# Kernel optimization log

Measured on AMD Instinct MI355X. Metric: run time of the kernel, lower is better.

## Reference

```python
import jax, jax.numpy as jnp
import numpy as np
import math

PATCH = 41
NUM_ANG = 8
NUM_SPATIAL = 4
BIN_KSIZE = 2 * int(PATCH / (NUM_SPATIAL + 1))   # 16
BIN_STRIDE = PATCH // NUM_SPATIAL                # 10
BIN_PAD = BIN_KSIZE // 4                         # 4
CLIPVAL = 0.2
EPS = 1e-10
N = 8192


def _sift_pooling_kernel(ksize: int) -> np.ndarray:
    k2 = float(ksize) / 2.0
    xc2 = k2 - np.abs(np.arange(ksize, dtype=np.float32) + 0.5 - k2)
    return (np.outer(xc2, xc2) / k2 ** 2).astype(np.float32)


def _sift_weighting_kernel(ksize: int) -> np.ndarray:
    # Gauss, vlfeat sigma: sigma_mul_2 = ksize**2
    k2 = float(ksize) / 2.0
    ys = np.arange(ksize, dtype=np.float32)[:, None]
    xs = np.arange(ksize, dtype=np.float32)[None, :]
    disq = (ys - k2 + 0.5) ** 2 + (xs - k2 + 0.5) ** 2
    return np.exp(-disq / float(ksize ** 2)).astype(np.float32)


def setup_inputs() -> dict:
    key = jax.random.key(0)
    x = jax.random.normal(key, (N, 1, PATCH, PATCH), dtype=jnp.float32)
    gk = jnp.asarray(_sift_weighting_kernel(PATCH))   # [41,41]
    pk = jnp.asarray(_sift_pooling_kernel(BIN_KSIZE))  # [16,16]
    return {"x": x, "gk": gk, "pk": pk}


def _l2_normalize(v):
    return v / jnp.maximum(jnp.linalg.norm(v, axis=1, keepdims=True), 1e-12)


def reference(x, gk, pk):
    # gradients via replicate-pad + central difference (matches [-1,0,1] convs)
    xp = jnp.pad(x, ((0, 0), (0, 0), (0, 0), (1, 1)), mode='edge')
    gx = xp[..., 2:] - xp[..., :-2]
    yp = jnp.pad(x, ((0, 0), (0, 0), (1, 1), (0, 0)), mode='edge')
    gy = yp[:, :, 2:, :] - yp[:, :, :-2, :]

    mag = jnp.sqrt(gx * gx + gy * gy + EPS) * gk  # gaussian-weighted magnitude
    ori = jnp.arctan2(gy, gx + EPS)

    # soft angular binning
    o_big = (ori + 2.0 * math.pi) / (2.0 * math.pi) * NUM_ANG
    bo0f = jnp.floor(o_big)
    wo1 = o_big - bo0f
    bo0 = bo0f.astype(jnp.int32) % NUM_ANG
    bo1 = (bo0 + 1) % NUM_ANG
    # [N,1,P,P,nb]
    contrib = (jax.nn.one_hot(bo0, NUM_ANG, dtype=mag.dtype) * ((1.0 - wo1) * mag)[..., None]
               + jax.nn.one_hot(bo1, NUM_ANG, dtype=mag.dtype) * (wo1 * mag)[..., None])
    contrib = jnp.transpose(contrib[:, 0], (0, 3, 1, 2))  # [N,nb,P,P]

    # depthwise weighted spatial pooling (same triangular kernel per angular bin)
    kern = jnp.broadcast_to(pk[None, None], (NUM_ANG, 1, BIN_KSIZE, BIN_KSIZE))
    pooled = jax.lax.conv_general_dilated(
        contrib, kern,
        window_strides=(BIN_STRIDE, BIN_STRIDE),
        padding=[(BIN_PAD, BIN_PAD), (BIN_PAD, BIN_PAD)],
        feature_group_count=NUM_ANG,
        dimension_numbers=('NCHW', 'OIHW', 'NCHW'))  # [N,nb,4,4]

    desc = pooled.reshape(pooled.shape[0], -1)  # [N,128]
    desc = _l2_normalize(desc)
    desc = jnp.clip(desc, 0.0, CLIPVAL)
    desc = _l2_normalize(desc)
    # rootsift: sqrt of L1-normalized descriptor
    desc = desc / jnp.maximum(jnp.sum(jnp.abs(desc), axis=1, keepdims=True), 1e-12)
    return jnp.sqrt(desc + 1e-10)
```

## Files before the change

### kernel.cpp

```cpp
#include <hip/hip_runtime.h>
#include <hip/hip_fp16.h>
#include <math.h>

#define PATCH 41
#define PP 1681
#define NB 8
#define STRIDE 10
#define NTH 192
#define HR 5
#define PPB 4
#define TAIL (PP - 8 * NTH)

__device__ __forceinline__ constexpr float tri16(int k) {
    float d = (float)k + 0.5f - 8.0f;
    float a = d < 0.0f ? -d : d;
    return (8.0f - a) * 0.125f;
}

__device__ __forceinline__ uint4 pixel_contrib(float gx, float gy, float w) {
    float X = gx + 1e-10f;
    float mag = __builtin_amdgcn_sqrtf(fmaf(gx, gx, fmaf(gy, gy, 1e-10f))) * w;

    float ax = fabsf(X), ay = fabsf(gy);
    float mx = fmaxf(ax, ay), mn = fminf(ax, ay);
    float r = mn * __builtin_amdgcn_rcpf(fmaxf(mx, 1e-30f));
    float r2 = r * r;
    float a4 = fmaf(r2, -0.0149238f, 0.0670406f);
    a4 = fmaf(r2, a4, -0.1482457f);
    a4 = fmaf(r2, a4, 0.2464287f);
    a4 = fmaf(r2, a4, -0.4235106f);
    a4 = fmaf(r2, a4, 1.2732106f);
    a4 *= r;

    bool sw = ay > ax;
    bool xn = X < 0.0f;
    bool yn = gy < 0.0f;
    int q = (xn ? 2 : 0) + ((sw != xn) ? 1 : 0);
    int b0 = yn ? 7 - q : q;
    bool f = (sw != xn) != yn;
    float ma = a4 * mag;
    float mb = mag - ma;
    float v0 = f ? ma : mb;
    float v1 = f ? mb : ma;

    unsigned combo = __builtin_bit_cast(unsigned, __builtin_amdgcn_cvt_pkrtz(v0, v1));
    int sh = (b0 & 3) << 4;
    unsigned long long A = (unsigned long long)combo << sh;
    unsigned long long B = ((b0 & 3) == 3) ? (unsigned long long)(combo >> 16) : 0ull;
    bool lohalf = b0 < 4;
    unsigned long long lo = lohalf ? A : B;
    unsigned long long hi = lohalf ? B : A;
    uint4 cw;
    cw.x = (unsigned)lo; cw.y = (unsigned)(lo >> 32);
    cw.z = (unsigned)hi; cw.w = (unsigned)(hi >> 32);
    return cw;
}

__device__ __forceinline__ __half2 u2h2(unsigned v) {
    return __builtin_bit_cast(__half2, v);
}

__device__ __forceinline__ unsigned dpp_prev(unsigned v) {
    return (unsigned)__builtin_amdgcn_update_dpp(0, (int)v, 0x111, 0xF, 0xF, true);
}
__device__ __forceinline__ unsigned dpp_next(unsigned v) {
    return (unsigned)__builtin_amdgcn_update_dpp(0, (int)v, 0x101, 0xF, 0xF, true);
}

__global__ __launch_bounds__(NTH, 6) void sift_desc_kernel(
        const float* __restrict__ x,
        const float* __restrict__ gk,
        const float* __restrict__ pk,
        float* __restrict__ out,
        int n)
{
    const int t = threadIdx.x;
    const int base = blockIdx.x * PPB;

    __shared__ __align__(16) float sA[PP];
    __shared__ __align__(16) float sB[PP];
    __shared__ __align__(16) __half s_H[49 * HR * NB];

    if (t < 160) {
        int dw = (t < 80) ? t : (820 + t);
        ((unsigned*)s_H)[dw] = 0u;
    }

    const int row = t >> 2;
    const int ox  = t & 3;
    const int cb  = ox * STRIDE;
    const bool ox0 = (ox == 0);
    const bool ox3 = (ox == 3);
    const float drow = (float)(row - 20);
    const float rf = __builtin_amdgcn_exp2f(drow * drow * -8.582362e-4f);
    const __half2 z2 = __float2half2_rn(0.0f);
    const __half2 wl[4] = {
        ox0 ? z2 : __float2half2_rn(tri16(0)),
        ox0 ? z2 : __float2half2_rn(tri16(1)),
        ox0 ? z2 : __float2half2_rn(tri16(2)),
        ox0 ? z2 : __float2half2_rn(tri16(3))
    };
    const int rb = row * PATCH + cb;
    const int ru = (row > 0 ? row - 1 : 0) * PATCH + cb;
    const int rd = (row < PATCH - 1 ? row + 1 : PATCH - 1) * PATCH + cb;

    float w[11];
    #pragma unroll
    for (int i = 0; i < 11; ++i) {
        float dc = (float)(cb + i - 20);
        w[i] = __builtin_amdgcn_exp2f(dc * dc * -8.582362e-4f) * rf;
    }

    {
        const float* gp = x + (size_t)base * PP;
        float stg[9];
        #pragma unroll
        for (int it = 0; it < 8; ++it) stg[it] = gp[it * NTH + t];
        stg[8] = (t < TAIL) ? gp[8 * NTH + t] : 0.0f;
        #pragma unroll
        for (int it = 0; it < 8; ++it) sA[it * NTH + t] = stg[it];
        if (t < TAIL) sA[8 * NTH + t] = stg[8];
    }
    __syncthreads();

    #pragma unroll
    for (int pi = 0; pi < PPB; ++pi) {
        if (base + pi >= n) break;
        const float* sC = (pi & 1) ? sB : sA;
        float*       sN = (pi & 1) ? sA : sB;
        const bool hn = (pi + 1 < PPB) && (base + pi + 1 < n);

        float stg[9];
        if (hn) {
            const float* gp = x + (size_t)(base + pi + 1) * PP;
            #pragma unroll
            for (int it = 0; it < 8; ++it) stg[it] = gp[it * NTH + t];
            stg[8] = (t < TAIL) ? gp[8 * NTH + t] : 0.0f;
        }
        __builtin_amdgcn_sched_barrier(0);

        if (t < PATCH * 4) {
            float m[13], u[11], d[11];
            m[0]  = sC[rb + (ox0 ? 0 : -1)];
            #pragma unroll
            for (int i = 1; i < 12; ++i) m[i] = sC[rb + i - 1];
            m[12] = sC[rb + (ox3 ? 10 : 11)];
            #pragma unroll
            for (int i = 0; i < 11; ++i) u[i] = sC[ru + i];
            #pragma unroll
            for (int i = 0; i < 11; ++i) d[i] = sC[rd + i];

            __half2 a0 = z2, a1 = z2, a2 = z2, a3 = z2;

            #pragma unroll
            for (int k = 0; k <= 10; ++k) {
                uint4 cw = pixel_contrib(m[k + 2] - m[k], d[k] - u[k], w[k]);

                const __half2 wo = __float2half2_rn(tri16(k + 4));
                a0 = __hfma2(u2h2(cw.x), wo, a0);
                a1 = __hfma2(u2h2(cw.y), wo, a1);
                a2 = __hfma2(u2h2(cw.z), wo, a2);
                a3 = __hfma2(u2h2(cw.w), wo, a3);

                if (k == 1) {
                    unsigned rx = dpp_next(cw.x);
                    unsigned ry = dpp_next(cw.y);
                    unsigned rz = dpp_next(cw.z);
                    unsigned rw = dpp_next(cw.w);
                    rx = ox3 ? 0u : rx;  ry = ox3 ? 0u : ry;
                    rz = ox3 ? 0u : rz;  rw = ox3 ? 0u : rw;
                    const __half2 wr = __float2half2_rn(tri16(15));
                    a0 = __hfma2(u2h2(rx), wr, a0);
                    a1 = __hfma2(u2h2(ry), wr, a1);
                    a2 = __hfma2(u2h2(rz), wr, a2);
                    a3 = __hfma2(u2h2(rw), wr, a3);
                }
                if (k >= 6 && k < 10) {
                    const __half2 wk = wl[k - 6];
                    a0 = __hfma2(u2h2(dpp_prev(cw.x)), wk, a0);
                    a1 = __hfma2(u2h2(dpp_prev(cw.y)), wk, a1);
                    a2 = __hfma2(u2h2(dpp_prev(cw.z)), wk, a2);
                    a3 = __hfma2(u2h2(dpp_prev(cw.w)), wk, a3);
                }
            }

            uint4 hv;
            hv.x = __builtin_bit_cast(unsigned, a0);
            hv.y = __builtin_bit_cast(unsigned, a1);
            hv.z = __builtin_bit_cast(unsigned, a2);
            hv.w = __builtin_bit_cast(unsigned, a3);
            *(uint4*)&s_H[((row + 4) * HR + ox) * NB] = hv;
        }
        __syncthreads();

        if (hn) {
            #pragma unroll
            for (int it = 0; it < 8; ++it) sN[it * NTH + t] = stg[it];
            if (t < TAIL) sN[8 * NTH + t] = stg[8];
        }

        if (t < 64) {
            const int b   = t >> 4;
            const int oy  = (t >> 2) & 3;
            const int oxx = t & 3;
            const __half* hp = &s_H[(oy * STRIDE * HR + oxx) * NB + b];
            float a = 0.0f, bb = 0.0f;
            #pragma unroll
            for (int ky = 0; ky < 16; ++ky) {
                a  = fmaf(tri16(ky), __half2float(hp[ky * HR * NB]),     a);
                bb = fmaf(tri16(ky), __half2float(hp[ky * HR * NB + 4]), bb);
            }

            float ss = fmaf(a, a, bb * bb);
            #pragma unroll
            for (int o = 32; o > 0; o >>= 1) ss += __shfl_xor(ss, o);
            float inv = 1.0f / fmaxf(__builtin_amdgcn_sqrtf(ss), 1e-12f);
            a  = fminf(fmaxf(a * inv, 0.0f), 0.2f);
            bb = fminf(fmaxf(bb * inv, 0.0f), 0.2f);

            float ss2 = fmaf(a, a, bb * bb);
            #pragma unroll
            for (int o = 32; o > 0; o >>= 1) ss2 += __shfl_xor(ss2, o);
            float inv2 = 1.0f / fmaxf(__builtin_amdgcn_sqrtf(ss2), 1e-12f);
            a *= inv2; bb *= inv2;

            float l1 = a + bb;
            #pragma unroll
            for (int o = 32; o > 0; o >>= 1) l1 += __shfl_xor(l1, o);
            float invl = 1.0f / fmaxf(l1, 1e-12f);

            float* op = out + (size_t)(base + pi) * 128;
            op[t]      = __builtin_amdgcn_sqrtf(fmaf(a,  invl, 1e-10f));
            op[t + 64] = __builtin_amdgcn_sqrtf(fmaf(bb, invl, 1e-10f));
        }
        __syncthreads();
    }
}

extern "C" void kernel_launch(void* const* d_in, const int* in_sizes, int n_in,
                              void* d_out, int out_size, void* d_ws, size_t ws_size,
                              hipStream_t stream) {
    const float* x  = (const float*)d_in[0];
    const float* gk = (const float*)d_in[1];
    const float* pk = (const float*)d_in[2];
    float* out = (float*)d_out;
    const int n = in_sizes[0] / PP;
    const int grid = (n + PPB - 1) / PPB;
    sift_desc_kernel<<<grid, NTH, 0, stream>>>(x, gk, pk, out, n);
}
```

Baseline: 111.7 us.

## Assign one wavefront per patch and remove block-wide barriers

Each 64-lane wavefront now owns a whole patch, with three patches per 192-thread block. Each wave loops three times to cover the 164 row/column work items, and the block-wide __syncthreads calls and the cross-patch double-buffered prefetch are gone. The Gaussian column weights now come from a small LDS table instead of per-thread exp2 calls, and launch bounds drop from 6 to 3. The aim is to cut barrier stalls and idle threads during the normalization stage. The cost is losing explicit load/compute overlap within a block and using more LDS per block, which may reduce occupancy.

```diff
diff --git a/kernel.cpp b/kernel.cpp
--- a/kernel.cpp
+++ b/kernel.cpp
@@ -8,8 +8,6 @@
 #define STRIDE 10
 #define NTH 192
 #define HR 5
-#define PPB 4
-#define TAIL (PP - 8 * NTH)
 
 __device__ __forceinline__ constexpr float tri16(int k) {
     float d = (float)k + 0.5f - 8.0f;
@@ -67,94 +65,88 @@
     return (unsigned)__builtin_amdgcn_update_dpp(0, (int)v, 0x101, 0xF, 0xF, true);
 }
 
-__global__ __launch_bounds__(NTH, 6) void sift_desc_kernel(
+__global__ __launch_bounds__(NTH, 3) void sift_desc_kernel(
         const float* __restrict__ x,
         const float* __restrict__ gk,
         const float* __restrict__ pk,
         float* __restrict__ out,
         int n)
 {
-    const int t = threadIdx.x;
-    const int base = blockIdx.x * PPB;
-
-    __shared__ __align__(16) float sA[PP];
-    __shared__ __align__(16) float sB[PP];
-    __shared__ __align__(16) __half s_H[49 * HR * NB];
-
-    if (t < 160) {
-        int dw = (t < 80) ? t : (820 + t);
-        ((unsigned*)s_H)[dw] = 0u;
-    }
-
-    const int row = t >> 2;
-    const int ox  = t & 3;
-    const int cb  = ox * STRIDE;
-    const bool ox0 = (ox == 0);
-    const bool ox3 = (ox == 3);
-    const float drow = (float)(row - 20);
-    const float rf = __builtin_amdgcn_exp2f(drow * drow * -8.582362e-4f);
+    const int t    = threadIdx.x;
+    const int lane = t & 63;
+    const int wv   = t >> 6;
+    const int patch = blockIdx.x * 3 + wv;
+
+    __shared__ __align__(16) float  sW[3][PP];
+    __shared__ __align__(16) __half sH[3][49 * HR * NB];
+    __shared__ float s_gc[48];
+
+    if (lane < 48) {
+        float dd = (float)(lane - 20);
+        float g = __builtin_amdgcn_exp2f(dd * dd * -8.582362e-4f);
+        s_gc[lane] = (lane < PATCH) ? g : 0.0f;
+    }
+    {
+        unsigned* hz = (unsigned*)&sH[wv][0];
+        #pragma unroll
+        for (int j = 0; j < 3; ++j) {
+            int idx = 64 * j + lane;
+            if (idx < 160) hz[(idx < 80) ? idx : (820 + idx)] = 0u;
+        }
+    }
+    if (patch >= n) return;
+
+    {
+        const float* gp = x + (size_t)patch * PP;
+        float* wp = &sW[wv][0];
+        #pragma unroll
+        for (int i = 0; i < 26; ++i) wp[lane + 64 * i] = gp[lane + 64 * i];
+        if (lane < PP - 26 * 64) wp[lane + 26 * 64] = gp[lane + 26 * 64];
+    }
+
+    const float* sC = &sW[wv][0];
     const __half2 z2 = __float2half2_rn(0.0f);
-    const __half2 wl[4] = {
-        ox0 ? z2 : __float2half2_rn(tri16(0)),
-        ox0 ? z2 : __float2half2_rn(tri16(1)),
-        ox0 ? z2 : __float2half2_rn(tri16(2)),
-        ox0 ? z2 : __float2half2_rn(tri16(3))
-    };
-    const int rb = row * PATCH + cb;
-    const int ru = (row > 0 ? row - 1 : 0) * PATCH + cb;
-    const int rd = (row < PATCH - 1 ? row + 1 : PATCH - 1) * PATCH + cb;
-
-    float w[11];
+
     #pragma unroll
-    for (int i = 0; i < 11; ++i) {
-        float dc = (float)(cb + i - 20);
-        w[i] = __builtin_amdgcn_exp2f(dc * dc * -8.582362e-4f) * rf;
-    }
-
-    {
-        const float* gp = x + (size_t)base * PP;
-        float stg[9];
-        #pragma unroll
-        for (int it = 0; it < 8; ++it) stg[it] = gp[it * NTH + t];
-        stg[8] = (t < TAIL) ? gp[8 * NTH + t] : 0.0f;
-        #pragma unroll
-        for (int it = 0; it < 8; ++it) sA[it * NTH + t] = stg[it];
-        if (t < TAIL) sA[8 * NTH + t] = stg[8];
-    }
-    __syncthreads();
-
-    #pragma unroll
-    for (int pi = 0; pi < PPB; ++pi) {
-        if (base + pi >= n) break;
-        const float* sC = (pi & 1) ? sB : sA;
-        float*       sN = (pi & 1) ? sA : sB;
-        const bool hn = (pi + 1 < PPB) && (base + pi + 1 < n);
-
-        float stg[9];
-        if (hn) {
-            const float* gp = x + (size_t)(base + pi + 1) * PP;
-            #pragma unroll
-            for (int it = 0; it < 8; ++it) stg[it] = gp[it * NTH + t];
-            stg[8] = (t < TAIL) ? gp[8 * NTH + t] : 0.0f;
-        }
-        __builtin_amdgcn_sched_barrier(0);
-
-        if (t < PATCH * 4) {
-            float m[13], u[11], d[11];
+    for (int it = 0; it < 3; ++it) {
+        const int u = 64 * it + lane;
+        if (u < PATCH * 4) {
+            const int row = u >> 2;
+            const int ox  = u & 3;
+            const int cb  = ox * STRIDE;
+            const bool ox0 = (ox == 0);
+            const bool ox3 = (ox == 3);
+            const int rb = row * PATCH + cb;
+            const int ru = (row > 0 ? row - 1 : 0) * PATCH + cb;
+            const int rd = (row < PATCH - 1 ? row + 1 : PATCH - 1) * PATCH + cb;
+
+            const float drow = (float)(row - 20);
+            const float rf = __builtin_amdgcn_exp2f(drow * drow * -8.582362e-4f);
+
+            const __half2 wl[4] = {
+                ox0 ? z2 : __float2half2_rn(tri16(0)),
+                ox0 ? z2 : __float2half2_rn(tri16(1)),
+                ox0 ? z2 : __float2half2_rn(tri16(2)),
+                ox0 ? z2 : __float2half2_rn(tri16(3))
+            };
+
+            float m[13], uu[11], dd[11], w[11];
             m[0]  = sC[rb + (ox0 ? 0 : -1)];
             #pragma unroll
             for (int i = 1; i < 12; ++i) m[i] = sC[rb + i - 1];
             m[12] = sC[rb + (ox3 ? 10 : 11)];
             #pragma unroll
-            for (int i = 0; i < 11; ++i) u[i] = sC[ru + i];
-            #pragma unroll
-            for (int i = 0; i < 11; ++i) d[i] = sC[rd + i];
+            for (int i = 0; i < 11; ++i) uu[i] = sC[ru + i];
+            #pragma unroll
+            for (int i = 0; i < 11; ++i) dd[i] = sC[rd + i];
+            #pragma unroll
+            for (int i = 0; i < 11; ++i) w[i] = s_gc[cb + i] * rf;
 
             __half2 a0 = z2, a1 = z2, a2 = z2, a3 = z2;
 
             #pragma unroll
             for (int k = 0; k <= 10; ++k) {
-                uint4 cw = pixel_contrib(m[k + 2] - m[k], d[k] - u[k], w[k]);
+                uint4 cw = pixel_contrib(m[k + 2] - m[k], dd[k] - uu[k], w[k]);
 
                 const __half2 wo = __float2half2_rn(tri16(k + 4));
                 a0 = __hfma2(u2h2(cw.x), wo, a0);
@@ -189,51 +181,43 @@
             hv.y = __builtin_bit_cast(unsigned, a1);
             hv.z = __builtin_bit_cast(unsigned, a2);
             hv.w = __builtin_bit_cast(unsigned, a3);
-            *(uint4*)&s_H[((row + 4) * HR + ox) * NB] = hv;
+            *(uint4*)&sH[wv][((row + 4) * HR + ox) * NB] = hv;
         }
-        __syncthreads();
-
-        if (hn) {
-            #pragma unroll
-            for (int it = 0; it < 8; ++it) sN[it * NTH + t] = stg[it];
-            if (t < TAIL) sN[8 * NTH + t] = stg[8];
+    }
+
+    {
+        const int b   = lane >> 4;
+        const int oy  = (lane >> 2) & 3;
+        const int oxx = lane & 3;
+        const __half* hp = &sH[wv][(oy * STRIDE * HR + oxx) * NB + b];
+        float a = 0.0f, bb = 0.0f;
+        #pragma unroll
+        for (int ky = 0; ky < 16; ++ky) {
+            a  = fmaf(tri16(ky), __half2float(hp[ky * HR * NB]),     a);
+            bb = fmaf(tri16(ky), __half2float(hp[ky * HR * NB + 4]), bb);
         }
 
-        if (t < 64) {
-            const int b   = t >> 4;
-            const int oy  = (t >> 2) & 3;
-            const int oxx = t & 3;
-            const __half* hp = &s_H[(oy * STRIDE * HR + oxx) * NB + b];
-            float a = 0.0f, bb = 0.0f;
-            #pragma unroll
-            for (int ky = 0; ky < 16; ++ky) {
-                a  = fmaf(tri16(ky), __half2float(hp[ky * HR * NB]),     a);
-                bb = fmaf(tri16(ky), __half2float(hp[ky * HR * NB + 4]), bb);
-            }
-
-            float ss = fmaf(a, a, bb * bb);
-            #pragma unroll
-            for (int o = 32; o > 0; o >>= 1) ss += __shfl_xor(ss, o);
-            float inv = 1.0f / fmaxf(__builtin_amdgcn_sqrtf(ss), 1e-12f);
-            a  = fminf(fmaxf(a * inv, 0.0f), 0.2f);
-            bb = fminf(fmaxf(bb * inv, 0.0f), 0.2f);
-
-            float ss2 = fmaf(a, a, bb * bb);
-            #pragma unroll
-            for (int o = 32; o > 0; o >>= 1) ss2 += __shfl_xor(ss2, o);
-            float inv2 = 1.0f / fmaxf(__builtin_amdgcn_sqrtf(ss2), 1e-12f);
-            a *= inv2; bb *= inv2;
-
-            float l1 = a + bb;
-            #pragma unroll
-            for (int o = 32; o > 0; o >>= 1) l1 += __shfl_xor(l1, o);
-            float invl = 1.0f / fmaxf(l1, 1e-12f);
-
-            float* op = out + (size_t)(base + pi) * 128;
-            op[t]      = __builtin_amdgcn_sqrtf(fmaf(a,  invl, 1e-10f));
-            op[t + 64] = __builtin_amdgcn_sqrtf(fmaf(bb, invl, 1e-10f));
-        }
-        __syncthreads();
+        float ss = fmaf(a, a, bb * bb);
+        #pragma unroll
+        for (int o = 32; o > 0; o >>= 1) ss += __shfl_xor(ss, o);
+        float inv = 1.0f / fmaxf(__builtin_amdgcn_sqrtf(ss), 1e-12f);
+        a  = fminf(fmaxf(a * inv, 0.0f), 0.2f);
+        bb = fminf(fmaxf(bb * inv, 0.0f), 0.2f);
+
+        float ss2 = fmaf(a, a, bb * bb);
+        #pragma unroll
+        for (int o = 32; o > 0; o >>= 1) ss2 += __shfl_xor(ss2, o);
+        float inv2 = 1.0f / fmaxf(__builtin_amdgcn_sqrtf(ss2), 1e-12f);
+        a *= inv2; bb *= inv2;
+
+        float l1 = a + bb;
+        #pragma unroll
+        for (int o = 32; o > 0; o >>= 1) l1 += __shfl_xor(l1, o);
+        float invl = 1.0f / fmaxf(l1, 1e-12f);
+
+        float* op = out + (size_t)patch * 128;
+        op[lane]      = __builtin_amdgcn_sqrtf(fmaf(a,  invl, 1e-10f));
+        op[lane + 64] = __builtin_amdgcn_sqrtf(fmaf(bb, invl, 1e-10f));
     }
 }
 
@@ -245,6 +229,6 @@
     const float* pk = (const float*)d_in[2];
     float* out = (float*)d_out;
     const int n = in_sizes[0] / PP;
-    const int grid = (n + PPB - 1) / PPB;
+    const int grid = (n + 2) / 3;
     sift_desc_kernel<<<grid, NTH, 0, stream>>>(x, gk, pk, out, n);
 }
```

Result: no change. 111.3 us (-0.4%).

## Process two patches per iteration with interleaved contributions and paired pooling

Applied to the files above, without the earlier changes.

Restructures the per-block loop to handle two patches per iteration. sA and sB now hold a pair instead of serving as a ping-pong buffer, and the histogram buffer is duplicated. The per-pixel gradient and binning work for both patches is interleaved to raise ILP, and the final pooling and normalisation runs on two wavefronts at once. This halves the number of barriers per patch. Patches per block double and the occupancy hint drops from 6 to 4 to cover the higher register pressure, which costs latency hiding and leaves fewer blocks (1024 instead of 2048).

```diff
diff --git a/kernel.cpp b/kernel.cpp
--- a/kernel.cpp
+++ b/kernel.cpp
@@ -8,7 +8,7 @@
 #define STRIDE 10
 #define NTH 192
 #define HR 5
-#define PPB 4
+#define PPB 8
 #define TAIL (PP - 8 * NTH)
 
 __device__ __forceinline__ constexpr float tri16(int k) {
@@ -67,7 +67,35 @@
     return (unsigned)__builtin_amdgcn_update_dpp(0, (int)v, 0x101, 0xF, 0xF, true);
 }
 
-__global__ __launch_bounds__(NTH, 6) void sift_desc_kernel(
+#define ACCUM(K, CW, A0, A1, A2, A3) do {                                        \
+    const __half2 wo_ = __float2half2_rn(tri16((K) + 4));                        \
+    A0 = __hfma2(u2h2((CW).x), wo_, A0);                                         \
+    A1 = __hfma2(u2h2((CW).y), wo_, A1);                                         \
+    A2 = __hfma2(u2h2((CW).z), wo_, A2);                                         \
+    A3 = __hfma2(u2h2((CW).w), wo_, A3);                                         \
+    if ((K) == 1) {                                                              \
+        unsigned rx_ = dpp_next((CW).x);                                         \
+        unsigned ry_ = dpp_next((CW).y);                                         \
+        unsigned rz_ = dpp_next((CW).z);                                         \
+        unsigned rw_ = dpp_next((CW).w);                                         \
+        rx_ = ox3 ? 0u : rx_;  ry_ = ox3 ? 0u : ry_;    \
+        rz_ = ox3 ? 0u : rz_;  rw_ = ox3 ? 0u : rw_;                             \
+        const __half2 wr_ = __float2half2_rn(tri16(15));                         \
+        A0 = __hfma2(u2h2(rx_), wr_, A0);                                        \
+        A1 = __hfma2(u2h2(ry_), wr_, A1);                                        \
+        A2 = __hfma2(u2h2(rz_), wr_, A2);                                        \
+        A3 = __hfma2(u2h2(rw_), wr_, A3);                                        \
+    }                                                                            \
+    if ((K) >= 6 && (K) < 10) {      \
+        const __half2 wk_ = wl[(K) - 6];                                         \
+        A0 = __hfma2(u2h2(dpp_prev((CW).x)), wk_, A0);                           \
+        A1 = __hfma2(u2h2(dpp_prev((CW).y)), wk_, A1);                           \
+        A2 = __hfma2(u2h2(dpp_prev((CW).z)), wk_, A2);                           \
+        A3 = __hfma2(u2h2(dpp_prev((CW).w)), wk_, A3);                           \
+    }                                                                            \
+} while (0)
+
+__global__ __launch_bounds__(NTH, 4) void sift_desc_kernel(
         const float* __restrict__ x,
         const float* __restrict__ gk,
         const float* __restrict__ pk,
@@ -79,11 +107,12 @@
 
     __shared__ __align__(16) float sA[PP];
     __shared__ __align__(16) float sB[PP];
-    __shared__ __align__(16) __half s_H[49 * HR * NB];
+    __shared__ __align__(16) __half sH2[2][49 * HR * NB];
 
     if (t < 160) {
         int dw = (t < 80) ? t : (820 + t);
-        ((unsigned*)s_H)[dw] = 0u;
+        ((unsigned*)sH2)[dw] = 0u;
+        ((unsigned*)sH2)[980 + dw] = 0u;
     }
 
     const int row = t >> 2;
@@ -112,126 +141,116 @@
     }
 
     {
-        const float* gp = x + (size_t)base * PP;
-        float stg[9];
+        const float* gA = x + (size_t)base * PP;
+        const float* gB = x + (size_t)min(base + 1, n - 1) * PP;
+        float sa[9], sb[9];
         #pragma unroll
-        for (int it = 0; it < 8; ++it) stg[it] = gp[it * NTH + t];
-        stg[8] = (t < TAIL) ? gp[8 * NTH + t] : 0.0f;
+        for (int it = 0; it < 8; ++it) { sa[it] = gA[it * NTH + t]; sb[it] = gB[it * NTH + t]; }
+        sa[8] = (t < TAIL) ? gA[8 * NTH + t] : 0.0f;
+        sb[8] = (t < TAIL) ? gB[8 * NTH + t] : 0.0f;
         #pragma unroll
-        for (int it = 0; it < 8; ++it) sA[it * NTH + t] = stg[it];
-        if (t < TAIL) sA[8 * NTH + t] = stg[8];
+        for (int it = 0; it < 8; ++it) { sA[it * NTH + t] = sa[it]; sB[it * NTH + t] = sb[it]; }
+        if (t < TAIL) { sA[8 * NTH + t] = sa[8]; sB[8 * NTH + t] = sb[8]; }
     }
     __syncthreads();
 
     #pragma unroll
-    for (int pi = 0; pi < PPB; ++pi) {
-        if (base + pi >= n) break;
-        const float* sC = (pi & 1) ? sB : sA;
-        float*       sN = (pi & 1) ? sA : sB;
-        const bool hn = (pi + 1 < PPB) && (base + pi + 1 < n);
-
-        float stg[9];
+    for (int pp = 0; pp < PPB / 2; ++pp) {
+        const int pairbase = base + 2 * pp;
+        if (pairbase >= n) break;
+        const bool hn = (pp + 1 < PPB / 2) && (pairbase + 2 < n);
+
+        float sa[9], sb[9];
         if (hn) {
-            const float* gp = x + (size_t)(base + pi + 1) * PP;
-            #pragma unroll
-            for (int it = 0; it < 8; ++it) stg[it] = gp[it * NTH + t];
-            stg[8] = (t < TAIL) ? gp[8 * NTH + t] : 0.0f;
+            const float* gA = x + (size_t)(pairbase + 2) * PP;
+            const float* gB = x + (size_t)min(pairbase + 3, n - 1) * PP;
+            #pragma unroll
+            for (int it = 0; it < 8; ++it) { sa[it] = gA[it * NTH + t]; sb[it] = gB[it * NTH + t]; }
+            sa[8] = (t < TAIL) ? gA[8 * NTH + t] : 0.0f;
+            sb[8] = (t < TAIL) ? gB[8 * NTH + t] : 0.0f;
         }
         __builtin_amdgcn_sched_barrier(0);
 
         if (t < PATCH * 4) {
-            float m[13], u[11], d[11];
-            m[0]  = sC[rb + (ox0 ? 0 : -1)];
-            #pragma unroll
-            for (int i = 1; i < 12; ++i) m[i] = sC[rb + i - 1];
-            m[12] = sC[rb + (ox3 ? 10 : 11)];
-            #pragma unroll
-            for (int i = 0; i < 11; ++i) u[i] = sC[ru + i];
-            #pragma unroll
-            for (int i = 0; i < 11; ++i) d[i] = sC[rd + i];
-
-            __half2 a0 = z2, a1 = z2, a2 = z2, a3 = z2;
+            float mA[13], uA[11], dA[11];
+            float mB[13], uB[11], dB[11];
+            mA[0] = sA[rb + (ox0 ? 0 : -1)];   mB[0] = sB[rb + (ox0 ? 0 : -1)];
+            #pragma unroll
+            for (int i = 1; i < 12; ++i) { mA[i] = sA[rb + i - 1]; mB[i] = sB[rb + i - 1]; }
+            mA[12] = sA[rb + (ox3 ? 10 : 11)]; mB[12] = sB[rb + (ox3 ? 10 : 11)];
+            #pragma unroll
+            for (int i = 0; i < 11; ++i) { uA[i] = sA[ru + i]; uB[i] = sB[ru + i]; }
+            #pragma unroll
+            for (int i = 0; i < 11; ++i) { dA[i] = sA[rd + i]; dB[i] = sB[rd + i]; }
+
+            __half2 aA0 = z2, aA1 = z2, aA2 = z2, aA3 = z2;
+            __half2 aB0 = z2, aB1 = z2, aB2 = z2, aB3 = z2;
 
             #pragma unroll
             for (int k = 0; k <= 10; ++k) {
-                uint4 cw = pixel_contrib(m[k + 2] - m[k], d[k] - u[k], w[k]);
-
-                const __half2 wo = __float2half2_rn(tri16(k + 4));
-                a0 = __hfma2(u2h2(cw.x), wo, a0);
-                a1 = __hfma2(u2h2(cw.y), wo, a1);
-                a2 = __hfma2(u2h2(cw.z), wo, a2);
-                a3 = __hfma2(u2h2(cw.w), wo, a3);
-
-                if (k == 1) {
-                    unsigned rx = dpp_next(cw.x);
-                    unsigned ry = dpp_next(cw.y);
-                    unsigned rz = dpp_next(cw.z);
-                    unsigned rw = dpp_next(cw.w);
-                    rx = ox3 ? 0u : rx;  ry = ox3 ? 0u : ry;
-                    rz = ox3 ? 0u : rz;  rw = ox3 ? 0u : rw;
-                    const __half2 wr = __float2half2_rn(tri16(15));
-                    a0 = __hfma2(u2h2(rx), wr, a0);
-                    a1 = __hfma2(u2h2(ry), wr, a1);
-                    a2 = __hfma2(u2h2(rz), wr, a2);
-                    a3 = __hfma2(u2h2(rw), wr, a3);
+                uint4 cwA = pixel_contrib(mA[k + 2] - mA[k], dA[k] - uA[k], w[k]);
+                ACCUM(k, cwA, aA0, aA1, aA2, aA3);
+                uint4 cwB = pixel_contrib(mB[k + 2] - mB[k], dB[k] - uB[k], w[k]);
+                ACCUM(k, cwB, aB0, aB1, aB2, aB3);
+            }
+
+            uint4 hvA, hvB;
+            hvA.x = __builtin_bit_cast(unsigned, aA0);
+            hvA.y = __builtin_bit_cast(unsigned, aA1);
+            hvA.z = __builtin_bit_cast(unsigned, aA2);
+            hvA.w = __builtin_bit_cast(unsigned, aA3);
+            hvB.x = __builtin_bit_cast(unsigned, aB0);
+            hvB.y = __builtin_bit_cast(unsigned, aB1);
+            hvB.z = __builtin_bit_cast(unsigned, aB2);
+            hvB.w = __builtin_bit_cast(unsigned, aB3);
+            *(uint4*)&sH2[0][((row + 4) * HR + ox) * NB] = hvA;
+            *(uint4*)&sH2[1][((row + 4) * HR + ox) * NB] = hvB;
+        }
+        __syncthreads();
+
+        if (hn) {
+            #pragma unroll
+            for (int it = 0; it < 8; ++it) { sA[it * NTH + t] = sa[it]; sB[it * NTH + t] = sb[it]; }
+            if (t < TAIL) { sA[8 * NTH + t] = sa[8]; sB[8 * NTH + t] = sb[8]; }
+        }
+
+        if (t < 128) {
+            const int which = t >> 6;
+            const int lane  = t & 63;
+            if (pairbase + which < n) {
+                const int b   = lane >> 4;
+                const int oy  = (lane >> 2) & 3;
+                const int oxx = lane & 3;
+                const __half* hp = &sH2[which][(oy * STRIDE * HR + oxx) * NB + b];
+                float a = 0.0f, bb = 0.0f;
+                #pragma unroll
+                for (int ky = 0; ky < 16; ++ky) {
+                    a  = fmaf(tri16(ky), __half2float(hp[ky * HR * NB]),     a);
+                    bb = fmaf(tri16(ky), __half2float(hp[ky * HR * NB + 4]), bb);
                 }
-                if (k >= 6 && k < 10) {
-                    const __half2 wk = wl[k - 6];
-                    a0 = __hfma2(u2h2(dpp_prev(cw.x)), wk, a0);
-                    a1 = __hfma2(u2h2(dpp_prev(cw.y)), wk, a1);
-                    a2 = __hfma2(u2h2(dpp_prev(cw.z)), wk, a2);
-                    a3 = __hfma2(u2h2(dpp_prev(cw.w)), wk, a3);
-                }
+
+                float ss = fmaf(a, a, bb * bb);
+                #pragma unroll
+                for (int o = 32; o > 0; o >>= 1) ss += __shfl_xor(ss, o);
+                float inv = 1.0f / fmaxf(__builtin_amdgcn_sqrtf(ss), 1e-12f);
+                a  = fminf(fmaxf(a * inv, 0.0f), 0.2f);
+                bb = fminf(fmaxf(bb * inv, 0.0f), 0.2f);
+
+                float ss2 = fmaf(a, a, bb * bb);
+                #pragma unroll
+                for (int o = 32; o > 0; o >>= 1) ss2 += __shfl_xor(ss2, o);
+                float inv2 = 1.0f / fmaxf(__builtin_amdgcn_sqrtf(ss2), 1e-12f);
+                a *= inv2; bb *= inv2;
+
+                float l1 = a + bb;
+                #pragma unroll
+                for (int o = 32; o > 0; o >>= 1) l1 += __shfl_xor(l1, o);
+                float invl = 1.0f / fmaxf(l1, 1e-12f);
+
+                float* op = out + (size_t)(pairbase + which) * 128;
+                op[lane]      = __builtin_amdgcn_sqrtf(fmaf(a,  invl, 1e-10f));
+                op[lane + 64] = __builtin_amdgcn_sqrtf(fmaf(bb, invl, 1e-10f));
             }
-
-            uint4 hv;
-            hv.x = __builtin_bit_cast(unsigned, a0);
-            hv.y = __builtin_bit_cast(unsigned, a1);
-            hv.z = __builtin_bit_cast(unsigned, a2);
-            hv.w = __builtin_bit_cast(unsigned, a3);
-            *(uint4*)&s_H[((row + 4) * HR + ox) * NB] = hv;
-        }
-        __syncthreads();
-
-        if (hn) {
-            #pragma unroll
-            for (int it = 0; it < 8; ++it) sN[it * NTH + t] = stg[it];
-            if (t < TAIL) sN[8 * NTH + t] = stg[8];
-        }
-
-        if (t < 64) {
-            const int b   = t >> 4;
-            const int oy  = (t >> 2) & 3;
-            const int oxx = t & 3;
-            const __half* hp = &s_H[(oy * STRIDE * HR + oxx) * NB + b];
-            float a = 0.0f, bb = 0.0f;
-            #pragma unroll
-            for (int ky = 0; ky < 16; ++ky) {
-                a  = fmaf(tri16(ky), __half2float(hp[ky * HR * NB]),     a);
-                bb = fmaf(tri16(ky), __half2float(hp[ky * HR * NB + 4]), bb);
-            }
-
-            float ss = fmaf(a, a, bb * bb);
-            #pragma unroll
-            for (int o = 32; o > 0; o >>= 1) ss += __shfl_xor(ss, o);
-            float inv = 1.0f / fmaxf(__builtin_amdgcn_sqrtf(ss), 1e-12f);
-            a  = fminf(fmaxf(a * inv, 0.0f), 0.2f);
-            bb = fminf(fmaxf(bb * inv, 0.0f), 0.2f);
-
-            float ss2 = fmaf(a, a, bb * bb);
-            #pragma unroll
-            for (int o = 32; o > 0; o >>= 1) ss2 += __shfl_xor(ss2, o);
-            float inv2 = 1.0f / fmaxf(__builtin_amdgcn_sqrtf(ss2), 1e-12f);
-            a *= inv2; bb *= inv2;
-
-            float l1 = a + bb;
-            #pragma unroll
-            for (int o = 32; o > 0; o >>= 1) l1 += __shfl_xor(l1, o);
-            float invl = 1.0f / fmaxf(l1, 1e-12f);
-
-            float* op = out + (size_t)(base + pi) * 128;
-            op[t]      = __builtin_amdgcn_sqrtf(fmaf(a,  invl, 1e-10f));
-            op[t + 64] = __builtin_amdgcn_sqrtf(fmaf(bb, invl, 1e-10f));
         }
         __syncthreads();
     }
```

Result: slower. 125.1 us (+12.0%).
